# Optimization experiments

Hardware: AMD Instinct MI355X
Metric: run time of the kernel (lower is better)

The kernel has to match this reference:

```python
import jax, jax.numpy as jnp
import numpy as np

EPS = 1e-13

def masked_softmax(x, mask):
    # Non-memory-efficient path of the original: softmax(x*mask), re-mask, renormalize.
    p = jax.nn.softmax(x * mask, axis=-1) * mask
    return p / (jnp.sum(p, axis=-1, keepdims=True) + EPS)

def setup_inputs() -> dict:
    key = jax.random.key(0)
    ka, kb, kma, kmb = jax.random.split(key, 4)
    B, La, Lb, D = 32, 1024, 1024, 256
    a = jax.random.normal(ka, (B, La, D), dtype=jnp.float32)
    b = jax.random.normal(kb, (B, Lb, D), dtype=jnp.float32)
    mask_a = jax.random.randint(kma, (B, La, 1), 0, 2, dtype=jnp.int32)
    mask_b = jax.random.randint(kmb, (B, Lb, 1), 0, 2, dtype=jnp.int32)
    return {"a": a, "b": b, "mask_a": mask_a, "mask_b": mask_b}

def reference(a, b, mask_a, mask_b):
    # a: [B, La, D], b: [B, Lb, D], mask_a: [B, La, 1], mask_b: [B, Lb, 1]
    ma = mask_a.astype(a.dtype)  # [B, La, 1]
    mb = mask_b.astype(b.dtype)  # [B, Lb, 1]
    attn = jnp.einsum('bid,bjd->bij', a, b)            # [B, La, Lb]
    amask = ma * jnp.swapaxes(mb, 1, 2)                 # outer product mask [B, La, Lb]
    weight_for_a = masked_softmax(attn, amask)          # softmax over Lb
    attended_a = jnp.einsum('bij,bjd->bid', weight_for_a, b)  # [B, La, D]
    attn_t = jnp.swapaxes(attn, 1, 2)                   # [B, Lb, La]
    amask_t = jnp.swapaxes(amask, 1, 2)
    weight_for_b = masked_softmax(attn_t, amask_t)      # softmax over La
    attended_b = jnp.einsum('bji,bid->bjd', weight_for_b, a)  # [B, Lb, D]
    return (attended_a, attended_b)
```

## Files before the change

### kernel.cpp

```cpp
#include <hip/hip_runtime.h>
#include <math.h>
#include <stdint.h>


#define NB    32
#define SEQ   1024
#define DIM   256
#define BM    128
#define BN    64
#define SHIFT 60.0f
#define PS    1048

typedef unsigned int uint;
typedef unsigned short ushort;
typedef __attribute__((ext_vector_type(8)))  short short8;
typedef __attribute__((ext_vector_type(16))) float f32x16;

#define KC_BATCH  (64 * 1024 * 8)
#define KC_TENSOR ((size_t)NB * KC_BATCH)
#define T_BATCH   (128 * 256 * 8)
#define T_TENSOR  ((size_t)NB * T_BATCH)
#define IDX_INTS  ((size_t)NB * SEQ)
#define WS_NEED   ((2 * KC_TENSOR + 2 * T_TENSOR) * sizeof(ushort) + (2 * IDX_INTS + 64) * sizeof(int))

__device__ __forceinline__ ushort bf16_rn(float x) {
    union { float f; uint u; } v; v.f = x;
    uint r = v.u + 0x7fffu + ((v.u >> 16) & 1u);
    return (ushort)(r >> 16);
}
__device__ __forceinline__ float bf16_to_f(ushort h) {
    union { uint u; float f; } v; v.u = ((uint)h) << 16;
    return v.f;
}
__device__ __forceinline__ void gl_lds16(const ushort* g, ushort* l) {
    __builtin_amdgcn_global_load_lds(
        (const __attribute__((address_space(1))) void*)g,
        (__attribute__((address_space(3))) void*)l, 16, 0, 0);
}

__global__ __launch_bounds__(1024)
void compact(const int* __restrict__ ma, const int* __restrict__ mb,
             int* __restrict__ idxA, int* __restrict__ idxB, int* __restrict__ nvArr)
{
    const int batch = blockIdx.x;
    const int t     = blockIdx.y;
    const int* m = t ? mb : ma;
    int* idx = (t ? idxB : idxA) + batch * SEQ;
    const int tid = threadIdx.x;
    const int lane = tid & 63, wv = tid >> 6;

    __shared__ int wsum[16];
    __shared__ int base[17];

    int v = (m[batch * SEQ + tid] != 0) ? 1 : 0;
    unsigned long long bal = __ballot(v);
    int lanePre = __popcll(bal & ((1ULL << lane) - 1ULL));
    if (lane == 0) wsum[wv] = __popcll(bal);
    __syncthreads();
    if (tid == 0) {
        int acc = 0;
        #pragma unroll
        for (int w = 0; w < 16; ++w) { base[w] = acc; acc += wsum[w]; }
        base[16] = acc;
        nvArr[t * NB + batch] = acc;
    }
    __syncthreads();
    if (v) idx[base[wv] + lanePre] = tid;
    if (tid >= base[16]) idx[tid] = 0;
}

__global__ __launch_bounds__(256)
void gatherK(const float* __restrict__ A, const float* __restrict__ Bt,
             const int* __restrict__ idxA, const int* __restrict__ idxB,
             const int* __restrict__ nvArr,
             ushort* __restrict__ aKc, ushort* __restrict__ bKc)
{
    const int z     = blockIdx.z;
    const int batch = blockIdx.y;
    const int soct  = blockIdx.x;
    const float* src = z ? Bt : A;
    const int* idx = (z ? idxB : idxA) + batch * SEQ;
    const int nv = nvArr[z * NB + batch];
    ushort* kcb = (z ? bKc : aKc) + (size_t)batch * KC_BATCH;

    const int tid = threadIdx.x;
    const int oct = tid >> 3, srow = tid & 7;
    const int c = soct * 8 + srow;

    float xs[8] = {0.f, 0.f, 0.f, 0.f, 0.f, 0.f, 0.f, 0.f};
    if (c < nv) {
        const float* rp = src + ((size_t)batch * SEQ + idx[c]) * DIM + oct * 8;
        float4 x0 = *(const float4*)rp;
        float4 x1 = *(const float4*)(rp + 4);
        xs[0]=x0.x; xs[1]=x0.y; xs[2]=x0.z; xs[3]=x0.w;
        xs[4]=x1.x; xs[5]=x1.y; xs[6]=x1.z; xs[7]=x1.w;
    }
    short8 hv, lv;
    #pragma unroll
    for (int j = 0; j < 8; ++j) {
        ushort h = bf16_rn(xs[j]);
        hv[j] = (short)h;
        lv[j] = (short)bf16_rn(xs[j] - bf16_to_f(h));
    }
    *(short8*)(kcb + (size_t)oct * 8192 + (size_t)c * 8)        = hv;
    *(short8*)(kcb + (size_t)(oct + 32) * 8192 + (size_t)c * 8) = lv;
}

__global__ __launch_bounds__(256)
void gatherT(const float* __restrict__ A, const float* __restrict__ Bt,
             const int* __restrict__ idxA, const int* __restrict__ idxB,
             const int* __restrict__ nvArr,
             ushort* __restrict__ aT, ushort* __restrict__ bT)
{
    const int z     = blockIdx.z;
    const int batch = blockIdx.y;
    const int soct  = blockIdx.x;
    const float* src = z ? Bt : A;
    const int* idx = (z ? idxB : idxA) + batch * SEQ;
    const int nv = nvArr[z * NB + batch];
    ushort* tp = (z ? bT : aT) + (size_t)batch * T_BATCH + (size_t)soct * 2048;
    const int d = threadIdx.x;
    short8 hv;
    #pragma unroll
    for (int j = 0; j < 8; ++j) {
        int c = soct * 8 + j;
        float x = 0.f;
        if (c < nv) x = src[((size_t)batch * SEQ + idx[c]) * DIM + d];
        hv[j] = (short)bf16_rn(x);
    }
    *(short8*)(tp + (size_t)d * 8) = hv;
}

__global__ __launch_bounds__(512, 2)
void attend3(const float*  __restrict__ A,   const float*  __restrict__ Bt,
             const ushort* __restrict__ aKc, const ushort* __restrict__ bKc,
             const ushort* __restrict__ aT,  const ushort* __restrict__ bT,
             const int*    __restrict__ nvArr,
             const int*    __restrict__ ma,  const int*    __restrict__ mb,
             float*        __restrict__ out)
{
    __shared__ __align__(16) ushort Ks2[64 * 512];
    __shared__ __align__(16) ushort Vt2[8 * 2048];
    __shared__ __align__(16) ushort Ph[8 * PS];
    __shared__ float lpart[2][BM];
    __shared__ float invs[BM];

    const int bx   = blockIdx.x;
    const int xcd  = bx & 7;
    const int slot = bx >> 3;
    const int rb   = slot & 7;
    const int pg   = slot >> 3;
    const int pair = xcd + 8 * pg;
    const int batch = pair >> 1;
    const int dir   = pair & 1;
    const int row0  = rb * BM;

    const float*  qsrc = dir ? Bt  : A;
    const ushort* kcY  = dir ? aKc : bKc;
    const ushort* tY   = dir ? aT  : bT;
    const int*    mx   = dir ? mb  : ma;
    const int     nv   = nvArr[(dir ? 0 : 1) * NB + batch];
    const int     ntiles = (nv + BN - 1) >> 6;
    float* o = out + (size_t)dir * NB * SEQ * DIM;

    const int tid  = threadIdx.x;
    const int lane = tid & 63;
    const int wave = tid >> 6;
    const int l31  = lane & 31;
    const int lh   = lane >> 5;
    const int rw   = wave >> 1;
    const int cw   = wave & 1;

    const ushort* kcYb = kcY + (size_t)batch * KC_BATCH;
    const ushort* tYb  = tY  + (size_t)batch * T_BATCH;

    const ushort* ksrc = kcYb + (size_t)(wave * 8) * 8192 + (size_t)lane * 8;
    ushort*       kdst = Ks2 + wave * 8 * 512 + lane * 8;
    const ushort* vsrc = tYb + (size_t)wave * 2048 + (size_t)lane * 8;
    ushort*       vdst = Vt2 + wave * 2048 + lane * 8;

    #pragma unroll
    for (int i = 0; i < 8; ++i) gl_lds16(ksrc + (size_t)i * 8192, kdst + i * 512);
    #pragma unroll
    for (int i = 0; i < 4; ++i) gl_lds16(vsrc + i * 512, vdst + i * 512);

    const int qrow = row0 + rw * 32 + l31;
    short8 qhi[16], qlo[16];
    {
        const float* qp = qsrc + ((size_t)batch * SEQ + qrow) * DIM + lh * 8;
        #pragma unroll
        for (int kk = 0; kk < 16; ++kk) {
            const float* p = qp + kk * 16;
            float4 x0 = *(const float4*)p;
            float4 x1 = *(const float4*)(p + 4);
            float xs[8] = {x0.x, x0.y, x0.z, x0.w, x1.x, x1.y, x1.z, x1.w};
            #pragma unroll
            for (int j = 0; j < 8; ++j) {
                ushort h = bf16_rn(xs[j]);
                qhi[kk][j] = (short)h;
                qlo[kk][j] = (short)bf16_rn(xs[j] - bf16_to_f(h));
            }
        }
    }

    f32x16 oacc[4];
    #pragma unroll
    for (int t = 0; t < 4; ++t)
        #pragma unroll
        for (int r = 0; r < 16; ++r) oacc[t][r] = 0.f;
    float lsum[16];
    #pragma unroll
    for (int r = 0; r < 16; ++r) lsum[r] = 0.f;

    __syncthreads();

    for (int nt = 0; nt < ntiles; ++nt) {
        const int key0 = nt * BN;
        const float mkv = (key0 + cw * 32 + l31 < nv) ? 1.f : 0.f;

        f32x16 a1, a2;
        #pragma unroll
        for (int r = 0; r < 16; ++r) { a1[r] = 0.f; a2[r] = 0.f; }
        const int kcol = (cw * 32 + l31) * 8;
        #pragma unroll
        for (int kk = 0; kk < 16; ++kk) {
            short8 bhi = *(const short8*)&Ks2[(2 * kk + lh) * 512 + kcol];
            a1 = __builtin_amdgcn_mfma_f32_32x32x16_bf16(qhi[kk], bhi, a1, 0, 0, 0);
            a2 = __builtin_amdgcn_mfma_f32_32x32x16_bf16(qlo[kk], bhi, a2, 0, 0, 0);
        }
        #pragma unroll
        for (int kk = 0; kk < 16; ++kk) {
            short8 blo = *(const short8*)&Ks2[(2 * kk + lh + 32) * 512 + kcol];
            a2 = __builtin_amdgcn_mfma_f32_32x32x16_bf16(qhi[kk], blo, a2, 0, 0, 0);
        }

        const int key  = cw * 32 + l31;
        const int koct = key >> 3, kj = key & 7;
        #pragma unroll
        for (int r = 0; r < 16; ++r) {
            float s = a1[r] + a2[r];
            float p = __expf(s - SHIFT) * mkv;
            lsum[r] += p;
            int qr = rw * 32 + (r & 3) + ((r >> 2) << 3) + (lh << 2);
            Ph[koct * PS + qr * 8 + kj] = bf16_rn(p);
        }
        __syncthreads();

        if (nt + 1 < ntiles) {
            const ushort* ks = ksrc + (size_t)(key0 + BN) * 8;
            #pragma unroll
            for (int i = 0; i < 8; ++i) gl_lds16(ks + (size_t)i * 8192, kdst + i * 512);
        }

        const int prow = (rw * 32 + l31) * 8;
        #pragma unroll
        for (int kb = 0; kb < 4; ++kb) {
            short8 pa = *(const short8*)&Ph[(2 * kb + lh) * PS + prow];
            #pragma unroll
            for (int t = 0; t < 4; ++t) {
                int dim = cw * 128 + t * 32 + l31;
                short8 vf = *(const short8*)&Vt2[(2 * kb + lh) * 2048 + dim * 8];
                oacc[t] = __builtin_amdgcn_mfma_f32_32x32x16_bf16(pa, vf, oacc[t], 0, 0, 0);
            }
        }
        __syncthreads();

        if (nt + 1 < ntiles) {
            const ushort* vs = vsrc + ((size_t)(key0 + BN) >> 3) * 2048;
            #pragma unroll
            for (int i = 0; i < 4; ++i) gl_lds16(vs + i * 512, vdst + i * 512);
        }
    }

    #pragma unroll
    for (int r = 0; r < 16; ++r) {
        float v = lsum[r];
        v += __shfl_xor(v, 1, 64);
        v += __shfl_xor(v, 2, 64);
        v += __shfl_xor(v, 4, 64);
        v += __shfl_xor(v, 8, 64);
        v += __shfl_xor(v, 16, 64);
        if (l31 == 0) {
            int row = rw * 32 + (r & 3) + ((r >> 2) << 3) + (lh << 2);
            lpart[cw][row] = v;
        }
    }
    __syncthreads();
    if (tid < BM) {
        float l = lpart[0][tid] + lpart[1][tid];
        int valid = mx[batch * SEQ + row0 + tid];
        invs[tid] = (valid != 0 && l > 0.f) ? 1.f / l : 0.f;
    }
    __syncthreads();

    float* ob = o + ((size_t)batch * SEQ + row0) * DIM;
    #pragma unroll
    for (int r = 0; r < 16; ++r) {
        int rloc = rw * 32 + (r & 3) + ((r >> 2) << 3) + (lh << 2);
        float inv = invs[rloc];
        #pragma unroll
        for (int t = 0; t < 4; ++t) {
            int d = cw * 128 + t * 32 + l31;
            ob[(size_t)rloc * DIM + d] = oacc[t][r] * inv;
        }
    }
}

#define F_KS_STR 520
#define F_P_STR  136
#define F_BM 64
#define F_BN 64
__global__ __launch_bounds__(256, 1)
void attend_mfma(const float* __restrict__ X, const float* __restrict__ Y,
                 const int* __restrict__ mx, const int* __restrict__ my,
                 float* __restrict__ out)
{
    __shared__ ushort Ks[F_BN * F_KS_STR];
    __shared__ ushort Ps[F_BM * F_P_STR];
    __shared__ float  mk[F_BN];
    __shared__ float  lpart[2][F_BM];
    __shared__ float  invs[F_BM];

    const int tid = threadIdx.x, lane = tid & 63, wave = tid >> 6;
    const int l31 = lane & 31, lh = lane >> 5;
    const int rw = wave >> 1, cw = wave & 1;
    const int batch = blockIdx.y, row0 = blockIdx.x * F_BM;
    const float* Xb = X + (size_t)batch * SEQ * DIM;
    const float* Yb = Y + (size_t)batch * SEQ * DIM;

    float4 kreg[16]; int mreg = 0;
    #pragma unroll
    for (int i = 0; i < 16; ++i) {
        int idx = tid + (i << 8); int r = idx >> 6, c4 = idx & 63;
        kreg[i] = *((const float4*)(Yb + (size_t)r * DIM) + c4);
    }
    if (tid < F_BN) mreg = my[batch * SEQ + tid];

    short8 qhi[16], qlo[16];
    {
        const float* qrow = Xb + (size_t)(row0 + rw * 32 + l31) * DIM + lh * 8;
        #pragma unroll
        for (int kk = 0; kk < 16; ++kk) {
            const float* p = qrow + kk * 16;
            float4 x0 = *(const float4*)p; float4 x1 = *(const float4*)(p + 4);
            float xs[8] = {x0.x, x0.y, x0.z, x0.w, x1.x, x1.y, x1.z, x1.w};
            #pragma unroll
            for (int j = 0; j < 8; ++j) {
                ushort h = bf16_rn(xs[j]);
                qhi[kk][j] = (short)h;
                qlo[kk][j] = (short)bf16_rn(xs[j] - bf16_to_f(h));
            }
        }
    }
    f32x16 oacc[4];
    #pragma unroll
    for (int t = 0; t < 4; ++t)
        #pragma unroll
        for (int r = 0; r < 16; ++r) oacc[t][r] = 0.f;
    float lsum[16];
    #pragma unroll
    for (int r = 0; r < 16; ++r) lsum[r] = 0.f;

    for (int nt = 0; nt < SEQ / F_BN; ++nt) {
        if (nt) __syncthreads();
        #pragma unroll
        for (int i = 0; i < 16; ++i) {
            int idx = tid + (i << 8); int r = idx >> 6, c4 = idx & 63;
            float f[4] = {kreg[i].x, kreg[i].y, kreg[i].z, kreg[i].w};
            ushort hh[4], ll[4];
            #pragma unroll
            for (int q = 0; q < 4; ++q) { hh[q] = bf16_rn(f[q]); ll[q] = bf16_rn(f[q] - bf16_to_f(hh[q])); }
            ushort4 hv; hv.x=hh[0];hv.y=hh[1];hv.z=hh[2];hv.w=hh[3];
            ushort4 lv; lv.x=ll[0];lv.y=ll[1];lv.z=ll[2];lv.w=ll[3];
            *(ushort4*)&Ks[r * F_KS_STR + c4 * 4] = hv;
            *(ushort4*)&Ks[r * F_KS_STR + 256 + c4 * 4] = lv;
        }
        if (tid < F_BN) mk[tid] = (float)mreg;
        __syncthreads();
        if (nt + 1 < SEQ / F_BN) {
            const float* Ybn = Yb + (size_t)(nt + 1) * F_BN * DIM;
            #pragma unroll
            for (int i = 0; i < 16; ++i) {
                int idx = tid + (i << 8); int r = idx >> 6, c4 = idx & 63;
                kreg[i] = *((const float4*)(Ybn + (size_t)r * DIM) + c4);
            }
            if (tid < F_BN) mreg = my[batch * SEQ + (nt + 1) * F_BN + tid];
        }
        f32x16 a1, a2, a3;
        #pragma unroll
        for (int r = 0; r < 16; ++r) { a1[r]=0.f; a2[r]=0.f; a3[r]=0.f; }
        const int krow = (cw * 32 + l31) * F_KS_STR;
        #pragma unroll
        for (int kk = 0; kk < 16; ++kk) {
            int col = kk * 16 + lh * 8;
            short8 bhi = *(const short8*)&Ks[krow + col];
            short8 blo = *(const short8*)&Ks[krow + 256 + col];
            a1 = __builtin_amdgcn_mfma_f32_32x32x16_bf16(qhi[kk], bhi, a1, 0, 0, 0);
            a2 = __builtin_amdgcn_mfma_f32_32x32x16_bf16(qlo[kk], bhi, a2, 0, 0, 0);
            a3 = __builtin_amdgcn_mfma_f32_32x32x16_bf16(qhi[kk], blo, a3, 0, 0, 0);
        }
        const float mkv = mk[cw * 32 + l31];
        #pragma unroll
        for (int r = 0; r < 16; ++r) {
            float s = a1[r] + a2[r] + a3[r];
            float p = __expf(s - SHIFT) * mkv;
            lsum[r] += p;
            ushort ph = bf16_rn(p);
            ushort pl = bf16_rn(p - bf16_to_f(ph));
            int prow = rw * 32 + (r & 3) + ((r >> 2) << 3) + (lh << 2);
            int pcol = cw * 32 + l31;
            Ps[prow * F_P_STR + pcol] = ph;
            Ps[prow * F_P_STR + 64 + pcol] = pl;
        }
        __syncthreads();
        const int prow = (rw * 32 + l31) * F_P_STR;
        #pragma unroll
        for (int kb = 0; kb < 4; ++kb) {
            int pcol = kb * 16 + lh * 8;
            short8 pa_hi = *(const short8*)&Ps[prow + pcol];
            short8 pa_lo = *(const short8*)&Ps[prow + 64 + pcol];
            #pragma unroll
            for (int t = 0; t < 4; ++t) {
                int d0 = cw * 128 + t * 32 + l31;
                short8 vf;
                #pragma unroll
                for (int j = 0; j < 8; ++j) vf[j] = (short)Ks[(pcol + j) * F_KS_STR + d0];
                oacc[t] = __builtin_amdgcn_mfma_f32_32x32x16_bf16(pa_hi, vf, oacc[t], 0, 0, 0);
                oacc[t] = __builtin_amdgcn_mfma_f32_32x32x16_bf16(pa_lo, vf, oacc[t], 0, 0, 0);
            }
        }
    }
    #pragma unroll
    for (int r = 0; r < 16; ++r) {
        float v = lsum[r];
        v += __shfl_xor(v, 1, 64); v += __shfl_xor(v, 2, 64); v += __shfl_xor(v, 4, 64);
        v += __shfl_xor(v, 8, 64); v += __shfl_xor(v, 16, 64);
        if (l31 == 0) {
            int row = rw * 32 + (r & 3) + ((r >> 2) << 3) + (lh << 2);
            lpart[cw][row] = v;
        }
    }
    __syncthreads();
    if (tid < F_BM) {
        float l = lpart[0][tid] + lpart[1][tid];
        int valid = mx[batch * SEQ + row0 + tid];
        invs[tid] = (valid != 0 && l > 0.f) ? 1.f / l : 0.f;
    }
    __syncthreads();
    float* ob = out + ((size_t)batch * SEQ + row0) * DIM;
    #pragma unroll
    for (int r = 0; r < 16; ++r) {
        int rloc = rw * 32 + (r & 3) + ((r >> 2) << 3) + (lh << 2);
        float inv = invs[rloc];
        #pragma unroll
        for (int t = 0; t < 4; ++t) {
            int d = cw * 128 + t * 32 + l31;
            ob[(size_t)rloc * DIM + d] = oacc[t][r] * inv;
        }
    }
}

extern "C" void kernel_launch(void* const* d_in, const int* in_sizes, int n_in,
                              void* d_out, int out_size, void* d_ws, size_t ws_size,
                              hipStream_t stream) {
    const float* a  = (const float*)d_in[0];
    const float* b  = (const float*)d_in[1];
    const int*   ma = (const int*)d_in[2];
    const int*   mb = (const int*)d_in[3];
    float* out = (float*)d_out;

    if (ws_size >= WS_NEED) {
        ushort* wsu = (ushort*)d_ws;
        ushort* aKc = wsu;
        ushort* bKc = wsu + KC_TENSOR;
        ushort* aT  = wsu + 2 * KC_TENSOR;
        ushort* bT  = wsu + 2 * KC_TENSOR + T_TENSOR;
        int* idxA  = (int*)(wsu + 2 * KC_TENSOR + 2 * T_TENSOR);
        int* idxB  = idxA + IDX_INTS;
        int* nvArr = idxB + IDX_INTS;

        compact<<<dim3(NB, 2), 1024, 0, stream>>>(ma, mb, idxA, idxB, nvArr);
        gatherK<<<dim3(128, NB, 2), 256, 0, stream>>>(a, b, idxA, idxB, nvArr, aKc, bKc);
        gatherT<<<dim3(128, NB, 2), 256, 0, stream>>>(a, b, idxA, idxB, nvArr, aT, bT);
        attend3<<<dim3(512, 1, 1), 512, 0, stream>>>(a, b, aKc, bKc, aT, bT,
                                                     nvArr, ma, mb, out);
    } else {
        float* out_a = out;
        float* out_b = out + (size_t)NB * SEQ * DIM;
        dim3 grid(SEQ / F_BM, NB), block(256);
        attend_mfma<<<grid, block, 0, stream>>>(a, b, ma, mb, out_a);
        attend_mfma<<<grid, block, 0, stream>>>(b, a, mb, ma, out_b);
    }
}
```

Baseline: 315.6 us.

## Compact query rows too, skip masked row blocks, and scatter outputs

```diff
diff --git a/kernel.cpp b/kernel.cpp
--- a/kernel.cpp
+++ b/kernel.cpp
@@ -131,12 +131,20 @@
     *(short8*)(tp + (size_t)d * 8) = hv;
 }
 
+__global__ __launch_bounds__(256)
+void zeroOut(float4* __restrict__ p, int n4)
+{
+    int i = blockIdx.x * 256 + threadIdx.x;
+    const int stride = gridDim.x * 256;
+    const float4 z = {0.f, 0.f, 0.f, 0.f};
+    for (; i < n4; i += stride) p[i] = z;
+}
+
 __global__ __launch_bounds__(512, 2)
-void attend3(const float*  __restrict__ A,   const float*  __restrict__ Bt,
-             const ushort* __restrict__ aKc, const ushort* __restrict__ bKc,
+void attend3(const ushort* __restrict__ aKc, const ushort* __restrict__ bKc,
              const ushort* __restrict__ aT,  const ushort* __restrict__ bT,
+             const int*    __restrict__ idxA, const int* __restrict__ idxB,
              const int*    __restrict__ nvArr,
-             const int*    __restrict__ ma,  const int*    __restrict__ mb,
              float*        __restrict__ out)
 {
     __shared__ __align__(16) ushort Ks2[64 * 512];
@@ -144,6 +152,7 @@
     __shared__ __align__(16) ushort Ph[8 * PS];
     __shared__ float lpart[2][BM];
     __shared__ float invs[BM];
+    __shared__ int   oidx[BM];
 
     const int bx   = blockIdx.x;
     const int xcd  = bx & 7;
@@ -155,13 +164,16 @@
     const int dir   = pair & 1;
     const int row0  = rb * BM;
 
-    const float*  qsrc = dir ? Bt  : A;
-    const ushort* kcY  = dir ? aKc : bKc;
-    const ushort* tY   = dir ? aT  : bT;
-    const int*    mx   = dir ? mb  : ma;
-    const int     nv   = nvArr[(dir ? 0 : 1) * NB + batch];
-    const int     ntiles = (nv + BN - 1) >> 6;
+    const ushort* qcY  = dir ? bKc  : aKc;
+    const ushort* kcY  = dir ? aKc  : bKc;
+    const ushort* tY   = dir ? aT   : bT;
+    const int*    idxX = dir ? idxB : idxA;
+    const int     nQ   = nvArr[(dir ? 1 : 0) * NB + batch];
+    const int     nK   = nvArr[(dir ? 0 : 1) * NB + batch];
+    const int     ntiles = (nK + BN - 1) >> 6;
     float* o = out + (size_t)dir * NB * SEQ * DIM;
+
+    if (row0 >= nQ) return;
 
     const int tid  = threadIdx.x;
     const int lane = tid & 63;
@@ -171,6 +183,7 @@
     const int rw   = wave >> 1;
     const int cw   = wave & 1;
 
+    const ushort* qcYb = qcY + (size_t)batch * KC_BATCH;
     const ushort* kcYb = kcY + (size_t)batch * KC_BATCH;
     const ushort* tYb  = tY  + (size_t)batch * T_BATCH;
 
@@ -187,19 +200,11 @@
     const int qrow = row0 + rw * 32 + l31;
     short8 qhi[16], qlo[16];
     {
-        const float* qp = qsrc + ((size_t)batch * SEQ + qrow) * DIM + lh * 8;
+        const ushort* qb = qcYb + (size_t)lh * 8192 + (size_t)qrow * 8;
         #pragma unroll
         for (int kk = 0; kk < 16; ++kk) {
-            const float* p = qp + kk * 16;
-            float4 x0 = *(const float4*)p;
-            float4 x1 = *(const float4*)(p + 4);
-            float xs[8] = {x0.x, x0.y, x0.z, x0.w, x1.x, x1.y, x1.z, x1.w};
-            #pragma unroll
-            for (int j = 0; j < 8; ++j) {
-                ushort h = bf16_rn(xs[j]);
-                qhi[kk][j] = (short)h;
-                qlo[kk][j] = (short)bf16_rn(xs[j] - bf16_to_f(h));
-            }
+            qhi[kk] = *(const short8*)(qb + (size_t)(2 * kk) * 8192);
+            qlo[kk] = *(const short8*)(qb + (size_t)(2 * kk + 32) * 8192);
         }
     }
 
@@ -216,7 +221,7 @@
 
     for (int nt = 0; nt < ntiles; ++nt) {
         const int key0 = nt * BN;
-        const float mkv = (key0 + cw * 32 + l31 < nv) ? 1.f : 0.f;
+        const float mkv = (key0 + cw * 32 + l31 < nK) ? 1.f : 0.f;
 
         f32x16 a1, a2;
         #pragma unroll
@@ -287,21 +292,26 @@
     }
     __syncthreads();
     if (tid < BM) {
+        int crow = row0 + tid;
         float l = lpart[0][tid] + lpart[1][tid];
-        int valid = mx[batch * SEQ + row0 + tid];
-        invs[tid] = (valid != 0 && l > 0.f) ? 1.f / l : 0.f;
-    }
-    __syncthreads();
-
-    float* ob = o + ((size_t)batch * SEQ + row0) * DIM;
+        int valid = (crow < nQ);
+        invs[tid] = (valid && l > 0.f) ? 1.f / l : 0.f;
+        oidx[tid] = valid ? idxX[batch * SEQ + crow] : 0;
+    }
+    __syncthreads();
+
+    float* ob = o + (size_t)batch * SEQ * DIM;
     #pragma unroll
     for (int r = 0; r < 16; ++r) {
         int rloc = rw * 32 + (r & 3) + ((r >> 2) << 3) + (lh << 2);
         float inv = invs[rloc];
-        #pragma unroll
-        for (int t = 0; t < 4; ++t) {
-            int d = cw * 128 + t * 32 + l31;
-            ob[(size_t)rloc * DIM + d] = oacc[t][r] * inv;
+        if (inv != 0.f) {
+            int orow = oidx[rloc];
+            #pragma unroll
+            for (int t = 0; t < 4; ++t) {
+                int d = cw * 128 + t * 32 + l31;
+                ob[(size_t)orow * DIM + d] = oacc[t][r] * inv;
+            }
         }
     }
 }
@@ -482,8 +492,9 @@
         compact<<<dim3(NB, 2), 1024, 0, stream>>>(ma, mb, idxA, idxB, nvArr);
         gatherK<<<dim3(128, NB, 2), 256, 0, stream>>>(a, b, idxA, idxB, nvArr, aKc, bKc);
         gatherT<<<dim3(128, NB, 2), 256, 0, stream>>>(a, b, idxA, idxB, nvArr, aT, bT);
-        attend3<<<dim3(512, 1, 1), 512, 0, stream>>>(a, b, aKc, bKc, aT, bT,
-                                                     nvArr, ma, mb, out);
+        zeroOut<<<dim3(2048), 256, 0, stream>>>((float4*)out, out_size / 16);
+        attend3<<<dim3(512, 1, 1), 512, 0, stream>>>(aKc, bKc, aT, bT,
+                                                     idxA, idxB, nvArr, out);
     } else {
         float* out_a = out;
         float* out_b = out + (size_t)NB * SEQ * DIM;
```

Measured after the change: 281.9 us. 1.12x faster.
